# Performance work log

Measured on AMD Instinct MI355X. Metric: run time of the kernel, lower is better.

The kernel has to match this reference:

```python
import jax, jax.numpy as jnp
import numpy as np

WINDOW_SIZE = 11
SIGMA = 1.5
CHANNELS = 3
DATA_RANGE = 1.0


def _create_window(window_size, channel):
    x = np.arange(window_size) - window_size // 2
    g = np.exp(-(x ** 2) / (2.0 * SIGMA ** 2))
    g = g / g.sum()
    w2d = np.outer(g, g).astype(np.float32)  # [ws, ws]
    # depthwise kernel, OIHW with I=1, O=channel
    return jnp.asarray(np.broadcast_to(w2d, (channel, 1, window_size, window_size)).copy())


def _depthwise_conv(x, window, channel):
    # x: [B, C, H, W], window: [C, 1, ws, ws], VALID padding, groups=C
    return jax.lax.conv_general_dilated(
        x, window, window_strides=(1, 1), padding='VALID',
        dimension_numbers=('NCHW', 'OIHW', 'NCHW'),
        feature_group_count=channel)


def setup_inputs() -> dict:
    key = jax.random.key(0)
    k1, k2 = jax.random.split(key)
    img1 = jax.random.uniform(k1, (32, CHANNELS, 512, 512), dtype=jnp.float32)
    img2 = jax.random.uniform(k2, (32, CHANNELS, 512, 512), dtype=jnp.float32)
    return {"img1": img1, "img2": img2}


def reference(img1, img2):
    channel = img1.shape[1]
    window = _create_window(WINDOW_SIZE, channel).astype(img1.dtype)

    mu1 = _depthwise_conv(img1, window, channel)
    mu2 = _depthwise_conv(img2, window, channel)
    mu1_sq = mu1 * mu1
    mu2_sq = mu2 * mu2
    mu1_mu2 = mu1 * mu2

    sigma1_sq = _depthwise_conv(img1 * img1, window, channel) - mu1_sq
    sigma2_sq = _depthwise_conv(img2 * img2, window, channel) - mu2_sq
    sigma12 = _depthwise_conv(img1 * img2, window, channel) - mu1_mu2

    C1 = (0.01 * DATA_RANGE) ** 2
    C2 = (0.03 * DATA_RANGE) ** 2
    v1 = 2.0 * sigma12 + C2
    v2 = sigma1_sq + sigma2_sq + C2
    ssim_map = (2.0 * mu1_mu2 + C1) * v1 / ((mu1_sq + mu2_sq + C1) * v2)
    # mean over channel, height, width -> per-image SSIM [B]
    return ssim_map.mean(axis=(1, 2, 3))
```

## Files before the change

kernel.cpp:

```cpp
#include <hip/hip_runtime.h>

#define H 512
#define W 512
#define OUT_Wc 502
#define OUT_Hc 502
#define C1c 1.0e-4f
#define C2c 9.0e-4f

#define TH 56
#define NR 66
#define RSTRIDE 128

__global__ __launch_bounds__(256, 4) void ssim_kernel(const float* __restrict__ img1,
                                                      const float* __restrict__ img2,
                                                      float* __restrict__ out) {
    __shared__ float2 ring[4][2][RSTRIDE];

    constexpr float GW[11] = {0.00102838f, 0.00759876f, 0.03600078f, 0.10936067f,
                              0.21300555f, 0.26601174f, 0.21300555f, 0.10936067f,
                              0.03600078f, 0.00759876f, 0.00102838f};

    const int tid  = threadIdx.x;
    const int wv   = tid >> 6;
    const int lane = tid & 63;

    const int plane = blockIdx.z;
    const size_t pbase = (size_t)plane * (H * W);
    const float* __restrict__ p1 = img1 + pbase;
    const float* __restrict__ p2 = img2 + pbase;

    const int Y0    = blockIdx.y * TH;
    const int wcol0 = (blockIdx.x * 4 + wv) * 64;
    const int gx    = wcol0 + lane;
    const int hx    = min(wcol0 + 64 + lane, W - 1);

    float2 (* __restrict__ wring)[RSTRIDE] = ring[wv];

    float acc0[11], acc1[11], acc2[11], acc3[11], acc4[11];
#pragma unroll
    for (int i = 0; i < 11; ++i) { acc0[i]=0.f; acc1[i]=0.f; acc2[i]=0.f; acc3[i]=0.f; acc4[i]=0.f; }

    const bool colok = (gx < OUT_Wc);
    float lsum = 0.f;

    float pa1[2], pa2[2], pb1[2], pb2[2];
    {
        const float* r0a = p1 + (size_t)Y0 * W;
        const float* r0b = p2 + (size_t)Y0 * W;
        pa1[0] = r0a[gx]; pa2[0] = r0b[gx];
        pb1[0] = r0a[hx]; pb2[0] = r0b[hx];
        const float* r1a = p1 + (size_t)(Y0 + 1) * W;
        const float* r1b = p2 + (size_t)(Y0 + 1) * W;
        pa1[1] = r1a[gx]; pa2[1] = r1b[gx];
        pb1[1] = r1a[hx]; pb2[1] = r1b[hx];
    }

#pragma unroll 1
    for (int rb = 0; rb < NR; rb += 11) {
#pragma unroll
        for (int p = 0; p < 11; ++p) {
            const int r = rb + p;
            const int slot = r & 1;

            wring[slot][lane]      = make_float2(pa1[slot], pa2[slot]);
            wring[slot][64 + lane] = make_float2(pb1[slot], pb2[slot]);

            {
                const int gy = min(Y0 + r + 2, H - 1);
                const float* __restrict__ n1 = p1 + (size_t)gy * W;
                const float* __restrict__ n2 = p2 + (size_t)gy * W;
                pa1[slot] = n1[gx]; pa2[slot] = n2[gx];
                pb1[slot] = n1[hx]; pb2[slot] = n2[hx];
            }

            __builtin_amdgcn_wave_barrier();

            float h0, h1, h2, h3, h4;
#pragma unroll
            for (int t = 0; t < 11; ++t) {
                const float2 v = wring[slot][lane + t];
                const float w = GW[t];
                if (t == 0) {
                    h0 = w * v.x;         h1 = w * v.y;
                    h2 = w * (v.x * v.x); h3 = w * (v.y * v.y);
                    h4 = w * (v.x * v.y);
                } else {
                    h0 = fmaf(w, v.x,       h0);
                    h1 = fmaf(w, v.y,       h1);
                    h2 = fmaf(w, v.x * v.x, h2);
                    h3 = fmaf(w, v.y * v.y, h3);
                    h4 = fmaf(w, v.x * v.y, h4);
                }
            }

#pragma unroll
            for (int a = 0; a < 11; ++a) {
                const float w = GW[(p - a + 11) % 11];
                if (a == p) {
                    acc0[a] = w * h0; acc1[a] = w * h1; acc2[a] = w * h2;
                    acc3[a] = w * h3; acc4[a] = w * h4;
                } else {
                    acc0[a] = fmaf(w, h0, acc0[a]);
                    acc1[a] = fmaf(w, h1, acc1[a]);
                    acc2[a] = fmaf(w, h2, acc2[a]);
                    acc3[a] = fmaf(w, h3, acc3[a]);
                    acc4[a] = fmaf(w, h4, acc4[a]);
                }
            }

            const int e = (p + 1) % 11;
            const int oy = Y0 + r - 10;
            if (r >= 10 && oy < OUT_Hc) {
                const float m1 = acc0[e], m2 = acc1[e];
                const float m12 = m1 * m2;
                const float sig12 = fmaf(-m1, m2, acc4[e]);
                const float num_a = fmaf(2.f, m12,   C1c);
                const float num_b = fmaf(2.f, sig12, C2c);
                const float den_a = fmaf(m1, m1, fmaf(m2, m2, C1c));
                const float den_b = (fmaf(-m1, m1, acc2[e]) + fmaf(-m2, m2, acc3[e])) + C2c;
                const float v = (num_a * num_b) * __builtin_amdgcn_rcpf(den_a * den_b);
                lsum += colok ? v : 0.f;
            }
        }
    }

#pragma unroll
    for (int off = 32; off > 0; off >>= 1) lsum += __shfl_down(lsum, off, 64);
    if (lane == 0) {
        const float inv_count = 1.0f / (3.0f * (float)OUT_Hc * (float)OUT_Wc);
        atomicAdd(&out[plane / 3], lsum * inv_count);
    }
}

__global__ void zero_out(float* out, int n) {
    int i = threadIdx.x + blockIdx.x * blockDim.x;
    if (i < n) out[i] = 0.f;
}

extern "C" void kernel_launch(void* const* d_in, const int* in_sizes, int n_in,
                              void* d_out, int out_size, void* d_ws, size_t ws_size,
                              hipStream_t stream) {
    const float* img1 = (const float*)d_in[0];
    const float* img2 = (const float*)d_in[1];
    float* out = (float*)d_out;

    zero_out<<<1, 64, 0, stream>>>(out, out_size);

    const int nplanes = in_sizes[0] / (H * W);
    dim3 grid(2,
              (OUT_Hc + TH - 1) / TH,
              nplanes);
    ssim_kernel<<<grid, 256, 0, stream>>>(img1, img2, out);
}
```

Baseline: 295.5 us.

## Use sum/difference transform and block-wide shared rows with deeper prefetch

Transforms pixel pairs into sum and difference, so only four filtered moments (s, d, s², d²) are needed instead of five, and the SSIM terms are rebuilt algebraically. The shared ring becomes one 266-wide row per block with a 4-slot ring, replacing per-wave 128-wide halos and cutting redundant halo loads. Two rows are processed per iteration behind a block-level __syncthreads, and global loads are prefetched four rows ahead. The cost is block-wide barriers in place of wave barriers, and a small risk from cancellation in the algebraic rewrite.

```diff
diff --git a/kernel.cpp b/kernel.cpp
--- a/kernel.cpp
+++ b/kernel.cpp
@@ -9,124 +9,141 @@
 
 #define TH 56
 #define NR 66
-#define RSTRIDE 128
+#define RW 266
+#define HALO 10
 
 __global__ __launch_bounds__(256, 4) void ssim_kernel(const float* __restrict__ img1,
                                                       const float* __restrict__ img2,
                                                       float* __restrict__ out) {
-    __shared__ float2 ring[4][2][RSTRIDE];
+    __shared__ float2 ring[4][RW];
 
     constexpr float GW[11] = {0.00102838f, 0.00759876f, 0.03600078f, 0.10936067f,
                               0.21300555f, 0.26601174f, 0.21300555f, 0.10936067f,
                               0.03600078f, 0.00759876f, 0.00102838f};
 
-    const int tid  = threadIdx.x;
-    const int wv   = tid >> 6;
-    const int lane = tid & 63;
-
+    const int tid = threadIdx.x;
+    const int X0 = blockIdx.x * 256;
+    const int Y0 = blockIdx.y * TH;
     const int plane = blockIdx.z;
     const size_t pbase = (size_t)plane * (H * W);
     const float* __restrict__ p1 = img1 + pbase;
     const float* __restrict__ p2 = img2 + pbase;
 
-    const int Y0    = blockIdx.y * TH;
-    const int wcol0 = (blockIdx.x * 4 + wv) * 64;
-    const int gx    = wcol0 + lane;
-    const int hx    = min(wcol0 + 64 + lane, W - 1);
+    const int gx = X0 + tid;
+    const int hx = min(X0 + 256 + tid, W - 1);
 
-    float2 (* __restrict__ wring)[RSTRIDE] = ring[wv];
-
-    float acc0[11], acc1[11], acc2[11], acc3[11], acc4[11];
+    float as_[11], ad_[11], aq_[11], ar_[11];
 #pragma unroll
-    for (int i = 0; i < 11; ++i) { acc0[i]=0.f; acc1[i]=0.f; acc2[i]=0.f; acc3[i]=0.f; acc4[i]=0.f; }
+    for (int i = 0; i < 11; ++i) { as_[i]=0.f; ad_[i]=0.f; aq_[i]=0.f; ar_[i]=0.f; }
 
     const bool colok = (gx < OUT_Wc);
     float lsum = 0.f;
 
-    float pa1[2], pa2[2], pb1[2], pb2[2];
+    float n0a, n0b, n1a, n1b, h0a, h0b, h1a, h1b;
+    float m0a, m0b, m1a, m1b, k0a, k0b, k1a, k1b;
     {
         const float* r0a = p1 + (size_t)Y0 * W;
         const float* r0b = p2 + (size_t)Y0 * W;
-        pa1[0] = r0a[gx]; pa2[0] = r0b[gx];
-        pb1[0] = r0a[hx]; pb2[0] = r0b[hx];
-        const float* r1a = p1 + (size_t)(Y0 + 1) * W;
-        const float* r1b = p2 + (size_t)(Y0 + 1) * W;
-        pa1[1] = r1a[gx]; pa2[1] = r1b[gx];
-        pb1[1] = r1a[hx]; pb2[1] = r1b[hx];
+        const float* r1a = r0a + W;
+        const float* r1b = r0b + W;
+        float x0a = r0a[gx], x0b = r0b[gx], x1a = r1a[gx], x1b = r1b[gx];
+        ring[0][tid] = make_float2(x0a + x0b, x0a - x0b);
+        ring[1][tid] = make_float2(x1a + x1b, x1a - x1b);
+        if (tid < HALO) {
+            float y0a = r0a[hx], y0b = r0b[hx], y1a = r1a[hx], y1b = r1b[hx];
+            ring[0][256 + tid] = make_float2(y0a + y0b, y0a - y0b);
+            ring[1][256 + tid] = make_float2(y1a + y1b, y1a - y1b);
+        }
+        const float* r2a = r0a + 2 * W;  const float* r2b = r0b + 2 * W;
+        const float* r3a = r0a + 3 * W;  const float* r3b = r0b + 3 * W;
+        const float* r4a = r0a + 4 * W;  const float* r4b = r0b + 4 * W;
+        const float* r5a = r0a + 5 * W;  const float* r5b = r0b + 5 * W;
+        n0a = r2a[gx]; n0b = r2b[gx]; n1a = r3a[gx]; n1b = r3b[gx];
+        m0a = r4a[gx]; m0b = r4b[gx]; m1a = r5a[gx]; m1b = r5b[gx];
+        h0a=h0b=h1a=h1b=k0a=k0b=k1a=k1b=0.f;
+        if (tid < HALO) {
+            h0a = r2a[hx]; h0b = r2b[hx]; h1a = r3a[hx]; h1b = r3b[hx];
+            k0a = r4a[hx]; k0b = r4b[hx]; k1a = r5a[hx]; k1b = r5b[hx];
+        }
+    }
+    __syncthreads();
+
+#define ROW_STEP(SLOT, PH, RRT)                                               \
+    {                                                                         \
+        const float2* __restrict__ rp = &ring[(SLOT)][tid];                   \
+        float hs, hd, hq, hr;                                                 \
+        _Pragma("unroll")                                                     \
+        for (int t = 0; t < 11; ++t) {                                        \
+            const float2 v = rp[t];                                           \
+            const float w = GW[t];                                            \
+            if (t == 0) { hs = w*v.x; hd = w*v.y;                             \
+                          hq = w*(v.x*v.x); hr = w*(v.y*v.y); }               \
+            else { hs = fmaf(w, v.x, hs); hd = fmaf(w, v.y, hd);              \
+                   hq = fmaf(w, v.x*v.x, hq); hr = fmaf(w, v.y*v.y, hr); }    \
+        }                                                                     \
+        _Pragma("unroll")                                                     \
+        for (int a = 0; a < 11; ++a) {                                        \
+            const float w = GW[((PH) - a + 11) % 11];                         \
+            if (a == (PH)) { as_[a]=w*hs; ad_[a]=w*hd; aq_[a]=w*hq; ar_[a]=w*hr; } \
+            else { as_[a]=fmaf(w,hs,as_[a]); ad_[a]=fmaf(w,hd,ad_[a]);        \
+                   aq_[a]=fmaf(w,hq,aq_[a]); ar_[a]=fmaf(w,hr,ar_[a]); }      \
+        }                                                                     \
+        const int e = ((PH) + 1) % 11;                                        \
+        const int oy = Y0 + (RRT) - 10;                                       \
+        if ((RRT) >= 10 && oy < OUT_Hc) {                                     \
+            const float ms = as_[e], md = ad_[e], qs = aq_[e], qd = ar_[e];   \
+            const float A = ms * ms, B = md * md;                             \
+            const float u = A - B, vv = A + B;                                \
+            const float w2 = qs - qd, z = qs + qd;                            \
+            const float num_a = fmaf(0.5f, u, C1c);                           \
+            const float den_a = fmaf(0.5f, vv, C1c);                          \
+            const float num_b = fmaf(0.5f, w2 - u, C2c);                      \
+            const float den_b = fmaf(0.5f, z - vv, C2c);                      \
+            const float val = (num_a * num_b) * __builtin_amdgcn_rcpf(den_a * den_b); \
+            lsum += colok ? val : 0.f;                                        \
+        }                                                                     \
     }
 
 #pragma unroll 1
-    for (int rb = 0; rb < NR; rb += 11) {
+    for (int rb = 0; rb < NR; rb += 22) {
 #pragma unroll
-        for (int p = 0; p < 11; ++p) {
+        for (int pp = 0; pp < 11; ++pp) {
+            const int p = 2 * pp;
             const int r = rb + p;
-            const int slot = r & 1;
 
-            wring[slot][lane]      = make_float2(pa1[slot], pa2[slot]);
-            wring[slot][64 + lane] = make_float2(pb1[slot], pb2[slot]);
+            const int gy6 = min(Y0 + r + 6, H - 1);
+            const int gy7 = min(Y0 + r + 7, H - 1);
+            const float* __restrict__ A6 = p1 + (size_t)gy6 * W;
+            const float* __restrict__ B6 = p2 + (size_t)gy6 * W;
+            const float* __restrict__ A7 = p1 + (size_t)gy7 * W;
+            const float* __restrict__ B7 = p2 + (size_t)gy7 * W;
+            const float t0a = A6[gx], t0b = B6[gx], t1a = A7[gx], t1b = B7[gx];
+            float u0a = 0.f, u0b = 0.f, u1a = 0.f, u1b = 0.f;
+            if (tid < HALO) { u0a = A6[hx]; u0b = B6[hx]; u1a = A7[hx]; u1b = B7[hx]; }
 
-            {
-                const int gy = min(Y0 + r + 2, H - 1);
-                const float* __restrict__ n1 = p1 + (size_t)gy * W;
-                const float* __restrict__ n2 = p2 + (size_t)gy * W;
-                pa1[slot] = n1[gx]; pa2[slot] = n2[gx];
-                pb1[slot] = n1[hx]; pb2[slot] = n2[hx];
+            const int s2 = (r + 2) & 3, s3 = (r + 3) & 3;
+            ring[s2][tid] = make_float2(n0a + n0b, n0a - n0b);
+            ring[s3][tid] = make_float2(n1a + n1b, n1a - n1b);
+            if (tid < HALO) {
+                ring[s2][256 + tid] = make_float2(h0a + h0b, h0a - h0b);
+                ring[s3][256 + tid] = make_float2(h1a + h1b, h1a - h1b);
             }
+            n0a = m0a; n0b = m0b; n1a = m1a; n1b = m1b;
+            h0a = k0a; h0b = k0b; h1a = k1a; h1b = k1b;
+            m0a = t0a; m0b = t0b; m1a = t1a; m1b = t1b;
+            k0a = u0a; k0b = u0b; k1a = u1a; k1b = u1b;
 
-            __builtin_amdgcn_wave_barrier();
+            ROW_STEP((r) & 3,     (2 * pp) % 11,     r);
+            ROW_STEP((r + 1) & 3, (2 * pp + 1) % 11, r + 1);
 
-            float h0, h1, h2, h3, h4;
-#pragma unroll
-            for (int t = 0; t < 11; ++t) {
-                const float2 v = wring[slot][lane + t];
-                const float w = GW[t];
-                if (t == 0) {
-                    h0 = w * v.x;         h1 = w * v.y;
-                    h2 = w * (v.x * v.x); h3 = w * (v.y * v.y);
-                    h4 = w * (v.x * v.y);
-                } else {
-                    h0 = fmaf(w, v.x,       h0);
-                    h1 = fmaf(w, v.y,       h1);
-                    h2 = fmaf(w, v.x * v.x, h2);
-                    h3 = fmaf(w, v.y * v.y, h3);
-                    h4 = fmaf(w, v.x * v.y, h4);
-                }
-            }
-
-#pragma unroll
-            for (int a = 0; a < 11; ++a) {
-                const float w = GW[(p - a + 11) % 11];
-                if (a == p) {
-                    acc0[a] = w * h0; acc1[a] = w * h1; acc2[a] = w * h2;
-                    acc3[a] = w * h3; acc4[a] = w * h4;
-                } else {
-                    acc0[a] = fmaf(w, h0, acc0[a]);
-                    acc1[a] = fmaf(w, h1, acc1[a]);
-                    acc2[a] = fmaf(w, h2, acc2[a]);
-                    acc3[a] = fmaf(w, h3, acc3[a]);
-                    acc4[a] = fmaf(w, h4, acc4[a]);
-                }
-            }
-
-            const int e = (p + 1) % 11;
-            const int oy = Y0 + r - 10;
-            if (r >= 10 && oy < OUT_Hc) {
-                const float m1 = acc0[e], m2 = acc1[e];
-                const float m12 = m1 * m2;
-                const float sig12 = fmaf(-m1, m2, acc4[e]);
-                const float num_a = fmaf(2.f, m12,   C1c);
-                const float num_b = fmaf(2.f, sig12, C2c);
-                const float den_a = fmaf(m1, m1, fmaf(m2, m2, C1c));
-                const float den_b = (fmaf(-m1, m1, acc2[e]) + fmaf(-m2, m2, acc3[e])) + C2c;
-                const float v = (num_a * num_b) * __builtin_amdgcn_rcpf(den_a * den_b);
-                lsum += colok ? v : 0.f;
-            }
+            __syncthreads();
         }
     }
+#undef ROW_STEP
 
 #pragma unroll
     for (int off = 32; off > 0; off >>= 1) lsum += __shfl_down(lsum, off, 64);
-    if (lane == 0) {
+    if ((tid & 63) == 0) {
         const float inv_count = 1.0f / (3.0f * (float)OUT_Hc * (float)OUT_Wc);
         atomicAdd(&out[plane / 3], lsum * inv_count);
     }
```

New measurement: 271.3 us. 8.2% less time.
